# Optimization experiments

Hardware: AMD Instinct MI355X
Metric: run time of the kernel (lower is better)

Reference implementation:

```python
import jax, jax.numpy as jnp
import numpy as np


def setup_inputs() -> dict:
    key = jax.random.key(0)
    k1, k2 = jax.random.split(key)
    B, L, V, D = 8, 2048, 1024, 1024
    hidden_states = jax.random.normal(k1, (B, L, D), dtype=jnp.float32)
    visual_hidden_state = jax.random.normal(k2, (B, V, D), dtype=jnp.float32)
    return {"hidden_states": hidden_states, "visual_hidden_state": visual_hidden_state}


def reference(hidden_states, visual_hidden_state):
    # fusion_scores = H @ V^T  (no scaling, no masking)
    scores = jnp.einsum("bld,bvd->blv", hidden_states, visual_hidden_state)
    probs = jax.nn.softmax(scores, axis=-1)
    # fusion_output = probs @ V
    return jnp.einsum("blv,bvd->bld", probs, visual_hidden_state)
```

## Files before the change

### kernel.cpp

```cpp
#include <hip/hip_runtime.h>


typedef _Float16 half8_t __attribute__((ext_vector_type(8)));
typedef _Float16 half4_t __attribute__((ext_vector_type(4)));
typedef __fp16   fp16x2  __attribute__((ext_vector_type(2)));
typedef float    f32x4   __attribute__((ext_vector_type(4)));

#define B_ 8
#define L_ 2048
#define V_ 1024
#define D_ 1024

__device__ __forceinline__ half8_t cvt8(f32x4 a, f32x4 b) {
  union { half8_t h; fp16x2 p[4]; } u;
  u.p[0] = __builtin_amdgcn_cvt_pkrtz(a[0], a[1]);
  u.p[1] = __builtin_amdgcn_cvt_pkrtz(a[2], a[3]);
  u.p[2] = __builtin_amdgcn_cvt_pkrtz(b[0], b[1]);
  u.p[3] = __builtin_amdgcn_cvt_pkrtz(b[2], b[3]);
  return u.h;
}
__device__ __forceinline__ half4_t cvt4(f32x4 a) {
  union { half4_t h; fp16x2 p[2]; } u;
  u.p[0] = __builtin_amdgcn_cvt_pkrtz(a[0], a[1]);
  u.p[1] = __builtin_amdgcn_cvt_pkrtz(a[2], a[3]);
  return u.h;
}

__device__ __forceinline__ void gload_lds16(const _Float16* g, _Float16* l) {
  __builtin_amdgcn_global_load_lds(
      (const __attribute__((address_space(1))) unsigned int*)(g),
      (__attribute__((address_space(3))) unsigned int*)(l), 16, 0, 0);
}

__global__ __launch_bounds__(256) void p0_hconv(const float* __restrict__ H,
                                                _Float16* __restrict__ Hh) {
  const size_t i = ((size_t)blockIdx.x * 256 + threadIdx.x) * 8;
  f32x4 a = *(const f32x4*)(H + i);
  f32x4 b = *(const f32x4*)(H + i + 4);
  *(half8_t*)(Hh + i) = cvt8(a, b);
}

__global__ __launch_bounds__(256) void p1_vconv(const float* __restrict__ V,
                                                _Float16* __restrict__ Vh,
                                                _Float16* __restrict__ VTh) {
  const int b  = blockIdx.z;
  const int d0 = blockIdx.x * 64;
  const int v0 = blockIdx.y * 64;
  const float* Vb = V + (size_t)b * V_ * D_;
  __shared__ __align__(16) _Float16 Lt[64 * 80];
  const int t   = threadIdx.x;
  const int dc4 = (t & 15) * 4;
  #pragma unroll
  for (int it = 0; it < 4; ++it) {
    const int vr = (t >> 4) + it * 16;
    f32x4 x = *(const f32x4*)(Vb + (size_t)(v0 + vr) * D_ + d0 + dc4);
    half4_t h = cvt4(x);
    *(half4_t*)(Vh + (size_t)b * V_ * D_ + (size_t)(v0 + vr) * D_ + d0 + dc4) = h;
    #pragma unroll
    for (int j = 0; j < 4; ++j) Lt[(dc4 + j) * 80 + vr] = h[j];
  }
  __syncthreads();
  #pragma unroll
  for (int it = 0; it < 2; ++it) {
    const int dr = (t >> 3) + it * 32;
    const int vc = (t & 7) * 8;
    half8_t y = *(const half8_t*)&Lt[dr * 80 + vc];
    *(half8_t*)(VTh + (size_t)b * D_ * V_ + (size_t)(d0 + dr) * V_ + v0 + vc) = y;
  }
}

#define PH_BAR() asm volatile("s_barrier" ::: "memory")

__global__ __launch_bounds__(512, 2) void gemm256(
    const _Float16* __restrict__ A, const _Float16* __restrict__ B,
    float* __restrict__ C) {
  int lin = blockIdx.x;
  lin = (lin & 7) * 32 + (lin >> 3);
  const int bz = lin >> 5;
  const int my = (lin >> 2) & 7;
  const int nx = lin & 3;
  const int m0 = my * 256, n0 = nx * 256;

  const _Float16* Ap = A + (size_t)bz * (2048 * 1024) + (size_t)m0 * 1024;
  const _Float16* Bp = B + (size_t)bz * (1024 * 1024) + (size_t)n0 * 1024;
  float*          Cp = C + (size_t)bz * (2048 * 1024);

  __shared__ __align__(16) _Float16 As[2][16384];
  __shared__ __align__(16) _Float16 Bs[2][16384];

  const int t    = threadIdx.x;
  const int lane = t & 63;
  const int wid  = t >> 6;
  const int wm   = wid >> 2;
  const int wn   = wid & 3;
  const int fr   = lane & 15;
  const int fk   = lane >> 4;

  f32x4 acc[8][4];
  {
    f32x4 z = {0.f, 0.f, 0.f, 0.f};
    #pragma unroll
    for (int i = 0; i < 8; ++i)
      #pragma unroll
      for (int j = 0; j < 4; ++j) acc[i][j] = z;
  }

  #define STG(PTR, ARR, BUFL, H, KTT)                                          \
    {                                                                          \
      _Pragma("unroll")                                                        \
      for (int i_ = 0; i_ < 2; ++i_) {                                         \
        const int c_ = i_ * 512 + t;                                           \
        const int kg_ = c_ >> 7, r_ = c_ & 127;                                \
        gload_lds16(PTR + (size_t)((H) * 128 + r_) * 1024 + (KTT) * 64 + kg_ * 8, \
                    &ARR[BUFL][(kg_ * 256 + (H) * 128 + r_) * 8]);             \
      }                                                                        \
    }

  #define LDA(BUFL, mt_, ks_) \
    (*(const half8_t*)&As[BUFL][(((ks_) * 4 + fk) * 256 + wm * 128 + (mt_) * 16 + fr) * 8])
  #define LDB(BUFL, nt_, ks_) \
    (*(const half8_t*)&Bs[BUFL][(((ks_) * 4 + fk) * 256 + wn * 64 + (nt_) * 16 + fr) * 8])

  #define MFMA16(AF, BF, MOFF, NOFF)                                           \
    __builtin_amdgcn_s_setprio(1);                                             \
    _Pragma("unroll")                                                          \
    for (int ks = 0; ks < 2; ++ks)                                             \
      _Pragma("unroll")                                                        \
      for (int nt = 0; nt < 2; ++nt)                                           \
        _Pragma("unroll")                                                      \
        for (int mt = 0; mt < 4; ++mt)                                         \
          acc[(MOFF) + mt][(NOFF) + nt] =                                      \
              __builtin_amdgcn_mfma_f32_16x16x32_f16(                          \
                  AF[mt][ks], BF[nt][ks], acc[(MOFF) + mt][(NOFF) + nt], 0, 0, 0); \
    __builtin_amdgcn_s_setprio(0);

  #define TILE(KT, BUFL)                                                       \
    {                                                                          \
      half8_t a[4][2], b0[2][2], b1[2][2];                                     \
                         \
      _Pragma("unroll")                                                        \
      for (int ks = 0; ks < 2; ++ks) {                                         \
        _Pragma("unroll")                                                      \
        for (int mt = 0; mt < 4; ++mt) a[mt][ks] = LDA(BUFL, mt, ks);          \
        _Pragma("unroll")                                                      \
        for (int nt = 0; nt < 2; ++nt) b0[nt][ks] = LDB(BUFL, nt, ks);         \
      }                                                                        \
      PH_BAR();                                                                \
      MFMA16(a, b0, 0, 0)                                                      \
      PH_BAR();                                                                \
                   \
      _Pragma("unroll")                                                        \
      for (int ks = 0; ks < 2; ++ks)                                           \
        _Pragma("unroll")                                                      \
        for (int nt = 0; nt < 2; ++nt) b1[nt][ks] = LDB(BUFL, 2 + nt, ks);     \
      if ((KT) < 14) { STG(Bp, Bs, BUFL, 0, (KT) + 2) }                        \
      PH_BAR();                                                                \
      MFMA16(a, b1, 0, 2)                                                      \
      PH_BAR();                                                                \
                   \
      _Pragma("unroll")                                                        \
      for (int ks = 0; ks < 2; ++ks)                                           \
        _Pragma("unroll")                                                      \
        for (int mt = 0; mt < 4; ++mt) a[mt][ks] = LDA(BUFL, 4 + mt, ks);      \
      if ((KT) < 14) { STG(Bp, Bs, BUFL, 1, (KT) + 2) }                        \
      PH_BAR();                                                                \
      MFMA16(a, b1, 4, 2)                                                      \
      PH_BAR();                                                                \
                \
      if ((KT) < 14) { STG(Ap, As, BUFL, 0, (KT) + 2) STG(Ap, As, BUFL, 1, (KT) + 2) } \
      PH_BAR();                                                                \
      MFMA16(a, b0, 4, 0)                                                      \
      if ((KT) <= 13) {                                                        \
        asm volatile("s_waitcnt vmcnt(8)" ::: "memory");                       \
      } else if ((KT) == 14) {                                                 \
        asm volatile("s_waitcnt vmcnt(0)" ::: "memory");                       \
      }                                                                        \
      PH_BAR();                                                                \
    }

  STG(Bp, Bs, 0, 0, 0) STG(Ap, As, 0, 0, 0) STG(Bp, Bs, 0, 1, 0) STG(Ap, As, 0, 1, 0)
  STG(Bp, Bs, 1, 0, 1) STG(Ap, As, 1, 0, 1) STG(Bp, Bs, 1, 1, 1) STG(Ap, As, 1, 1, 1)
  asm volatile("s_waitcnt vmcnt(8)" ::: "memory");
  PH_BAR();

  #pragma unroll 1
  for (int ktp = 0; ktp < 8; ++ktp) {
    TILE(2 * ktp, 0)
    TILE(2 * ktp + 1, 1)
  }
  #undef TILE
  #undef STG
  #undef LDA
  #undef LDB
  #undef MFMA16

  const int rq = (lane >> 4) * 4;
  const int cb = n0 + wn * 64 + (lane & 15);
  const int rb = m0 + wm * 128 + rq;
  #pragma unroll
  for (int mt = 0; mt < 8; ++mt)
    #pragma unroll
    for (int nt = 0; nt < 4; ++nt) {
      #pragma unroll
      for (int r = 0; r < 4; ++r)
        Cp[(size_t)(rb + mt * 16 + r) * 1024 + cb + nt * 16] = acc[mt][nt][r];
    }
}

__global__ __launch_bounds__(256) void k2_softmax(const float* __restrict__ S,
                                                  _Float16* __restrict__ P) {
  const int t    = threadIdx.x;
  const int lane = t & 63;
  const int row  = blockIdx.x * 4 + (t >> 6);
  const float* Sr = S + (size_t)row * V_;

  f32x4 s[4];
  #pragma unroll
  for (int j = 0; j < 4; ++j) s[j] = *(const f32x4*)(Sr + (lane + 64 * j) * 4);

  float m = -1e30f;
  #pragma unroll
  for (int j = 0; j < 4; ++j)
    m = fmaxf(m, fmaxf(fmaxf(s[j][0], s[j][1]), fmaxf(s[j][2], s[j][3])));
  #pragma unroll
  for (int off = 1; off < 64; off <<= 1) m = fmaxf(m, __shfl_xor(m, off, 64));

  float sum = 0.f;
  #pragma unroll
  for (int j = 0; j < 4; ++j) {
    s[j][0] = __expf(s[j][0] - m); s[j][1] = __expf(s[j][1] - m);
    s[j][2] = __expf(s[j][2] - m); s[j][3] = __expf(s[j][3] - m);
    sum += (s[j][0] + s[j][1]) + (s[j][2] + s[j][3]);
  }
  #pragma unroll
  for (int off = 1; off < 64; off <<= 1) sum += __shfl_xor(sum, off, 64);
  const float inv = 1.0f / sum;

  _Float16* Pr = P + (size_t)row * V_;
  #pragma unroll
  for (int j = 0; j < 4; ++j) {
    f32x4 e = {s[j][0] * inv, s[j][1] * inv, s[j][2] * inv, s[j][3] * inv};
    *(half4_t*)(Pr + (lane + 64 * j) * 4) = cvt4(e);
  }
}

__global__ __launch_bounds__(256, 2) void k1_slow(
    const float* __restrict__ H, const float* __restrict__ Vv, float* __restrict__ S) {
  const int b  = blockIdx.z;
  const int m0 = blockIdx.y * 128;
  const int n0 = blockIdx.x * 128;
  const float* Hb = H  + (size_t)b * L_ * D_;
  const float* Vb = Vv + (size_t)b * V_ * D_;
  float*       Sb = S  + (size_t)b * L_ * V_;
  __shared__ __align__(16) _Float16 As[2][4096];
  __shared__ __align__(16) _Float16 Bs[2][4096];
  const int t = threadIdx.x, lane = t & 63, wm = (t >> 6) >> 1, wn = (t >> 6) & 1;
  f32x4 acc[4][4];
  { f32x4 z = {0,0,0,0};
    #pragma unroll
    for (int i = 0; i < 4; ++i)
      #pragma unroll
      for (int j = 0; j < 4; ++j) acc[i][j] = z; }
  const int skg = t & 3, sm = t >> 2;
  for (int kt = 0; kt < 32; ++kt) {
    const int kbase = kt * 32 + skg * 8, buf = kt & 1;
    #pragma unroll
    for (int h = 0; h < 2; ++h) {
      const int m = sm + h * 64;
      const float* sa = Hb + (size_t)(m0 + m) * D_ + kbase;
      const float* sb = Vb + (size_t)(n0 + m) * D_ + kbase;
      const int cell = skg * 128 + (m ^ (skg * 2));
      *(half8_t*)&As[buf][cell * 8] = cvt8(*(const f32x4*)sa, *(const f32x4*)(sa + 4));
      *(half8_t*)&Bs[buf][cell * 8] = cvt8(*(const f32x4*)sb, *(const f32x4*)(sb + 4));
    }
    __syncthreads();
    const int fkg = lane >> 4, fr = lane & 15;
    half8_t af[4];
    #pragma unroll
    for (int mt = 0; mt < 4; ++mt)
      af[mt] = *(const half8_t*)&As[buf][(fkg * 128 + ((wm * 64 + mt * 16 + fr) ^ (fkg * 2))) * 8];
    #pragma unroll
    for (int nt = 0; nt < 4; ++nt) {
      half8_t bf = *(const half8_t*)&Bs[buf][(fkg * 128 + ((wn * 64 + nt * 16 + fr) ^ (fkg * 2))) * 8];
      #pragma unroll
      for (int mt = 0; mt < 4; ++mt)
        acc[mt][nt] = __builtin_amdgcn_mfma_f32_16x16x32_f16(af[mt], bf, acc[mt][nt], 0, 0, 0);
    }
  }
  const int rq = (lane >> 4) * 4;
  #pragma unroll
  for (int mt = 0; mt < 4; ++mt)
    #pragma unroll
    for (int nt = 0; nt < 4; ++nt) {
      const int col = n0 + wn * 64 + nt * 16 + (lane & 15);
      const int rb  = m0 + wm * 64 + mt * 16 + rq;
      #pragma unroll
      for (int r = 0; r < 4; ++r) Sb[(size_t)(rb + r) * V_ + col] = acc[mt][nt][r];
    }
}

__global__ __launch_bounds__(256) void k2_slow(float* __restrict__ S) {
  const int row = blockIdx.x;
  float* Sr = S + (size_t)row * V_;
  const int t = threadIdx.x;
  f32x4 s = ((const f32x4*)Sr)[t];
  float m = fmaxf(fmaxf(s[0], s[1]), fmaxf(s[2], s[3]));
  #pragma unroll
  for (int off = 1; off < 64; off <<= 1) m = fmaxf(m, __shfl_xor(m, off, 64));
  __shared__ float redm[4];
  __shared__ float reds[4];
  const int w = t >> 6;
  if ((t & 63) == 0) redm[w] = m;
  __syncthreads();
  m = fmaxf(fmaxf(redm[0], redm[1]), fmaxf(redm[2], redm[3]));
  const float e0 = __expf(s[0] - m), e1 = __expf(s[1] - m);
  const float e2 = __expf(s[2] - m), e3 = __expf(s[3] - m);
  float sum = (e0 + e1) + (e2 + e3);
  #pragma unroll
  for (int off = 1; off < 64; off <<= 1) sum += __shfl_xor(sum, off, 64);
  if ((t & 63) == 0) reds[w] = sum;
  __syncthreads();
  const float inv = 1.0f / ((reds[0] + reds[1]) + (reds[2] + reds[3]));
  half4_t p;
  p[0] = (_Float16)(e0 * inv); p[1] = (_Float16)(e1 * inv);
  p[2] = (_Float16)(e2 * inv); p[3] = (_Float16)(e3 * inv);
  *(half4_t*)((_Float16*)Sr + 4 * t) = p;
}

__global__ __launch_bounds__(512, 2) void k3_slow(
    const float* __restrict__ Vv, float* __restrict__ O) {
  const int b = blockIdx.y, r0 = blockIdx.x * 64;
  const float* Vb = Vv + (size_t)b * V_ * D_;
  float*       Ob = O  + (size_t)b * L_ * D_;
  const _Float16* Pb = (const _Float16*)Ob;
  __shared__ __align__(16) _Float16 Bs[32768];
  const int t = threadIdx.x, lane = t & 63, w = t >> 6;
  f32x4 acc[4][8];
  { f32x4 z = {0,0,0,0};
    #pragma unroll
    for (int i = 0; i < 4; ++i)
      #pragma unroll
      for (int j = 0; j < 8; ++j) acc[i][j] = z; }
  for (int kt = 0; kt < 32; ++kt) {
    const int v0 = kt * 32;
    #pragma unroll
    for (int i = 0; i < 8; ++i) {
      const int c = t + i * 512, kg = c >> 10, d = c & 1023;
      const float* src = Vb + (size_t)(v0 + kg * 8) * D_ + d;
      f32x4 x0, x1;
      x0[0] = src[0*D_]; x0[1] = src[1*D_]; x0[2] = src[2*D_]; x0[3] = src[3*D_];
      x1[0] = src[4*D_]; x1[1] = src[5*D_]; x1[2] = src[6*D_]; x1[3] = src[7*D_];
      *(half8_t*)&Bs[(kg * 1024 + d) * 8] = cvt8(x0, x1);
    }
    __syncthreads();
    const int fkg = lane >> 4, fr = lane & 15;
    half8_t af[4];
    #pragma unroll
    for (int mt = 0; mt < 4; ++mt)
      af[mt] = *(const half8_t*)(Pb + (size_t)(r0 + mt * 16 + fr) * 2048 + v0 + fkg * 8);
    #pragma unroll
    for (int nt = 0; nt < 8; ++nt) {
      half8_t bf = *(const half8_t*)&Bs[(fkg * 1024 + w * 128 + nt * 16 + fr) * 8];
      #pragma unroll
      for (int mt = 0; mt < 4; ++mt)
        acc[mt][nt] = __builtin_amdgcn_mfma_f32_16x16x32_f16(af[mt], bf, acc[mt][nt], 0, 0, 0);
    }
    __syncthreads();
  }
  const int rq = (lane >> 4) * 4;
  #pragma unroll
  for (int mt = 0; mt < 4; ++mt)
    #pragma unroll
    for (int nt = 0; nt < 8; ++nt) {
      const int col = w * 128 + nt * 16 + (lane & 15);
      const int rb  = r0 + mt * 16 + rq;
      #pragma unroll
      for (int r = 0; r < 4; ++r) Ob[(size_t)(rb + r) * D_ + col] = acc[mt][nt][r];
    }
}

extern "C" void kernel_launch(void* const* d_in, const int* in_sizes, int n_in,
                              void* d_out, int out_size, void* d_ws, size_t ws_size,
                              hipStream_t stream) {
  (void)in_sizes; (void)n_in; (void)out_size;
  const float* H  = (const float*)d_in[0];
  const float* Vv = (const float*)d_in[1];
  float* O = (float*)d_out;

  const size_t need = (size_t)64 * 1024 * 1024;
  if (ws_size >= need && d_ws != nullptr) {
    _Float16* Hh  = (_Float16*)d_ws;
    _Float16* Vh  = Hh + (size_t)B_ * L_ * D_;
    _Float16* VTh = Vh + (size_t)B_ * V_ * D_;
    _Float16* P   = Hh;

    p0_hconv<<<dim3((B_ * L_ * D_) / (256 * 8)), 256, 0, stream>>>(H, Hh);
    p1_vconv<<<dim3(D_ / 64, V_ / 64, B_), 256, 0, stream>>>(Vv, Vh, VTh);
    gemm256<<<dim3(256), 512, 0, stream>>>(Hh, Vh, O);
    k2_softmax<<<dim3(B_ * L_ / 4), 256, 0, stream>>>(O, P);
    gemm256<<<dim3(256), 512, 0, stream>>>(P, VTh, O);
  } else {
    k1_slow<<<dim3(V_ / 128, L_ / 128, B_), 256, 0, stream>>>(H, Vv, O);
    k2_slow<<<dim3(B_ * L_), 256, 0, stream>>>(O);
    k3_slow<<<dim3(L_ / 64, B_), 512, 0, stream>>>(Vv, O);
  }
}
```

Measured before the change: 255.0 us.

## Prefetch next k-tile LDS fragments, stage GEMM epilogue via LDS, merge conversion kernels

Restructures the GEMM main loop so the A-low and B0 fragments for the next k-tile are read from the other LDS buffer during the current tile, with ping-pong register sets and sched_barriers so LDS reads overlap MFMA work. It also loosens the vmcnt wait. The epilogue now stages accumulators through LDS and writes C with coalesced 16-byte row stores instead of scattered scalar stores. The two fp32-to-fp16 conversion kernels are merged into one launch to save a kernel launch. The cost is higher register pressure from the extra fragment sets and added barriers in the epilogue.

New measurement: 284.4 us. 11.5% more time.

```diff
diff --git a/kernel.cpp b/kernel.cpp
--- a/kernel.cpp
+++ b/kernel.cpp
@@ -32,23 +32,25 @@
       (__attribute__((address_space(3))) unsigned int*)(l), 16, 0, 0);
 }
 
-__global__ __launch_bounds__(256) void p0_hconv(const float* __restrict__ H,
-                                                _Float16* __restrict__ Hh) {
-  const size_t i = ((size_t)blockIdx.x * 256 + threadIdx.x) * 8;
-  f32x4 a = *(const f32x4*)(H + i);
-  f32x4 b = *(const f32x4*)(H + i + 4);
-  *(half8_t*)(Hh + i) = cvt8(a, b);
-}
-
-__global__ __launch_bounds__(256) void p1_vconv(const float* __restrict__ V,
+__global__ __launch_bounds__(256) void p01_conv(const float* __restrict__ H,
+                                                _Float16* __restrict__ Hh,
+                                                const float* __restrict__ V,
                                                 _Float16* __restrict__ Vh,
                                                 _Float16* __restrict__ VTh) {
-  const int b  = blockIdx.z;
-  const int d0 = blockIdx.x * 64;
-  const int v0 = blockIdx.y * 64;
+  const int t = threadIdx.x;
+  if (blockIdx.x < 8192) {
+    const size_t i = ((size_t)blockIdx.x * 256 + t) * 8;
+    f32x4 a = *(const f32x4*)(H + i);
+    f32x4 b = *(const f32x4*)(H + i + 4);
+    *(half8_t*)(Hh + i) = cvt8(a, b);
+    return;
+  }
+  const int lin = blockIdx.x - 8192;
+  const int b   = lin >> 8;
+  const int d0  = (lin & 15) * 64;
+  const int v0  = ((lin >> 4) & 15) * 64;
   const float* Vb = V + (size_t)b * V_ * D_;
   __shared__ __align__(16) _Float16 Lt[64 * 80];
-  const int t   = threadIdx.x;
   const int dc4 = (t & 15) * 4;
   #pragma unroll
   for (int it = 0; it < 4; ++it) {
@@ -68,8 +70,6 @@
     *(half8_t*)(VTh + (size_t)b * D_ * V_ + (size_t)(d0 + dr) * V_ + v0 + vc) = y;
   }
 }
-
-#define PH_BAR() asm volatile("s_barrier" ::: "memory")
 
 __global__ __launch_bounds__(512, 2) void gemm256(
     const _Float16* __restrict__ A, const _Float16* __restrict__ B,
@@ -134,59 +134,70 @@
                   AF[mt][ks], BF[nt][ks], acc[(MOFF) + mt][(NOFF) + nt], 0, 0, 0); \
     __builtin_amdgcn_s_setprio(0);
 
-  #define TILE(KT, BUFL)                                                       \
+  half8_t aLo[4][2], aHi[4][2], b1[2][2], b0A[2][2], b0B[2][2];
+
+  #define TILE(KT, BUFL, OTH, B0C, B0N)                                        \
     {                                                                          \
-      half8_t a[4][2], b0[2][2], b1[2][2];                                     \
-                         \
-      _Pragma("unroll")                                                        \
-      for (int ks = 0; ks < 2; ++ks) {                                         \
-        _Pragma("unroll")                                                      \
-        for (int mt = 0; mt < 4; ++mt) a[mt][ks] = LDA(BUFL, mt, ks);          \
-        _Pragma("unroll")                                                      \
-        for (int nt = 0; nt < 2; ++nt) b0[nt][ks] = LDB(BUFL, nt, ks);         \
-      }                                                                        \
-      PH_BAR();                                                                \
-      MFMA16(a, b0, 0, 0)                                                      \
-      PH_BAR();                                                                \
-                   \
+                                 \
       _Pragma("unroll")                                                        \
       for (int ks = 0; ks < 2; ++ks)                                           \
         _Pragma("unroll")                                                      \
         for (int nt = 0; nt < 2; ++nt) b1[nt][ks] = LDB(BUFL, 2 + nt, ks);     \
-      if ((KT) < 14) { STG(Bp, Bs, BUFL, 0, (KT) + 2) }                        \
-      PH_BAR();                                                                \
-      MFMA16(a, b1, 0, 2)                                                      \
-      PH_BAR();                                                                \
-                   \
+      __builtin_amdgcn_sched_barrier(0);                                       \
+      MFMA16(aLo, B0C, 0, 0)                                                   \
+      __builtin_amdgcn_s_barrier();                                            \
+                      \
       _Pragma("unroll")                                                        \
       for (int ks = 0; ks < 2; ++ks)                                           \
         _Pragma("unroll")                                                      \
-        for (int mt = 0; mt < 4; ++mt) a[mt][ks] = LDA(BUFL, 4 + mt, ks);      \
+        for (int mt = 0; mt < 4; ++mt) aHi[mt][ks] = LDA(BUFL, 4 + mt, ks);    \
+      if ((KT) < 14) { STG(Bp, Bs, BUFL, 0, (KT) + 2) }                        \
+      __builtin_amdgcn_sched_barrier(0);                                       \
+      MFMA16(aLo, b1, 0, 2)                                                    \
+      __builtin_amdgcn_s_barrier();                                            \
+                       \
       if ((KT) < 14) { STG(Bp, Bs, BUFL, 1, (KT) + 2) }                        \
-      PH_BAR();                                                                \
-      MFMA16(a, b1, 4, 2)                                                      \
-      PH_BAR();                                                                \
-                \
+      __builtin_amdgcn_sched_barrier(0);                                       \
+      MFMA16(aHi, b1, 4, 2)                                                    \
+      if ((KT) == 14) {                                                        \
+        asm volatile("s_waitcnt vmcnt(0)" ::: "memory");                       \
+      } else if ((KT) < 14) {                                                  \
+        asm volatile("s_waitcnt vmcnt(4)" ::: "memory");                       \
+      }                                                                        \
+      __builtin_amdgcn_s_barrier();                                            \
+             \
+      if ((KT) < 15) {                                                         \
+        _Pragma("unroll")                                                      \
+        for (int ks = 0; ks < 2; ++ks) {                                       \
+          _Pragma("unroll")                                                    \
+          for (int mt = 0; mt < 4; ++mt) aLo[mt][ks] = LDA(OTH, mt, ks);       \
+          _Pragma("unroll")                                                    \
+          for (int nt = 0; nt < 2; ++nt) B0N[nt][ks] = LDB(OTH, nt, ks);       \
+        }                                                                      \
+      }                                                                        \
       if ((KT) < 14) { STG(Ap, As, BUFL, 0, (KT) + 2) STG(Ap, As, BUFL, 1, (KT) + 2) } \
-      PH_BAR();                                                                \
-      MFMA16(a, b0, 4, 0)                                                      \
-      if ((KT) <= 13) {                                                        \
-        asm volatile("s_waitcnt vmcnt(8)" ::: "memory");                       \
-      } else if ((KT) == 14) {                                                 \
-        asm volatile("s_waitcnt vmcnt(0)" ::: "memory");                       \
-      }                                                                        \
-      PH_BAR();                                                                \
+      __builtin_amdgcn_sched_barrier(0);                                       \
+      MFMA16(aHi, B0C, 4, 0)                                                   \
+      __builtin_amdgcn_s_barrier();                                            \
     }
 
   STG(Bp, Bs, 0, 0, 0) STG(Ap, As, 0, 0, 0) STG(Bp, Bs, 0, 1, 0) STG(Ap, As, 0, 1, 0)
   STG(Bp, Bs, 1, 0, 1) STG(Ap, As, 1, 0, 1) STG(Bp, Bs, 1, 1, 1) STG(Ap, As, 1, 1, 1)
   asm volatile("s_waitcnt vmcnt(8)" ::: "memory");
-  PH_BAR();
+  __builtin_amdgcn_s_barrier();
+  #pragma unroll
+  for (int ks = 0; ks < 2; ++ks) {
+    #pragma unroll
+    for (int mt = 0; mt < 4; ++mt) aLo[mt][ks] = LDA(0, mt, ks);
+    #pragma unroll
+    for (int nt = 0; nt < 2; ++nt) b0A[nt][ks] = LDB(0, nt, ks);
+  }
 
   #pragma unroll 1
-  for (int ktp = 0; ktp < 8; ++ktp) {
-    TILE(2 * ktp, 0)
-    TILE(2 * ktp + 1, 1)
+  for (int tp = 0; tp < 8; ++tp) {
+    const int kt = tp * 2;
+    TILE(kt, 0, 1, b0A, b0B)
+    TILE(kt + 1, 1, 0, b0B, b0A)
   }
   #undef TILE
   #undef STG
@@ -195,16 +206,26 @@
   #undef MFMA16
 
   const int rq = (lane >> 4) * 4;
-  const int cb = n0 + wn * 64 + (lane & 15);
-  const int rb = m0 + wm * 128 + rq;
-  #pragma unroll
-  for (int mt = 0; mt < 8; ++mt)
-    #pragma unroll
-    for (int nt = 0; nt < 4; ++nt) {
-      #pragma unroll
-      for (int r = 0; r < 4; ++r)
-        Cp[(size_t)(rb + mt * 16 + r) * 1024 + cb + nt * 16] = acc[mt][nt][r];
-    }
+  float* reg = (wid < 4) ? ((float*)As + wid * 4096)
+                         : ((float*)Bs + (wid - 4) * 4096);
+  #pragma unroll
+  for (int h = 0; h < 2; ++h) {
+    __syncthreads();
+    #pragma unroll
+    for (int mt = 0; mt < 4; ++mt)
+      #pragma unroll
+      for (int nt = 0; nt < 4; ++nt)
+        #pragma unroll
+        for (int r = 0; r < 4; ++r)
+          reg[(mt * 16 + rq + r) * 64 + nt * 16 + fr] = acc[h * 4 + mt][nt][r];
+    __syncthreads();
+    #pragma unroll
+    for (int rr = 0; rr < 16; ++rr) {
+      f32x4 v = *(const f32x4*)&reg[(rr * 4 + fk) * 64 + fr * 4];
+      const int row = m0 + wm * 128 + h * 64 + rr * 4 + fk;
+      *(f32x4*)&Cp[(size_t)row * 1024 + n0 + wn * 64 + fr * 4] = v;
+    }
+  }
 }
 
 __global__ __launch_bounds__(256) void k2_softmax(const float* __restrict__ S,
@@ -394,8 +415,7 @@
     _Float16* VTh = Vh + (size_t)B_ * V_ * D_;
     _Float16* P   = Hh;
 
-    p0_hconv<<<dim3((B_ * L_ * D_) / (256 * 8)), 256, 0, stream>>>(H, Hh);
-    p1_vconv<<<dim3(D_ / 64, V_ / 64, B_), 256, 0, stream>>>(Vv, Vh, VTh);
+    p01_conv<<<dim3(8192 + 2048), 256, 0, stream>>>(H, Hh, Vv, Vh, VTh);
     gemm256<<<dim3(256), 512, 0, stream>>>(Hh, Vh, O);
     k2_softmax<<<dim3(B_ * L_ / 4), 256, 0, stream>>>(O, P);
     gemm256<<<dim3(256), 512, 0, stream>>>(P, VTh, O);
```

## Fuse conversion, both GEMMs and softmax into one persistent kernel with grid barriers

Applied to the files above, without the earlier changes.

Replaces five separate launches (H conversion, V conversion/transpose, GEMM, softmax, GEMM) with a single persistent 256-block kernel that runs each phase in turn, separated by atomic-counter grid barriers. The aim is to remove launch gaps and per-kernel tail effects. In exchange it adds global spin barriers and a memset of the barrier counters before every launch. It also relies on all 256 blocks being co-resident, and softmax and conversion now run on only 256 blocks instead of many small ones.

Result: slower. 498.0 us (+95.3%).

```diff
diff --git a/kernel.cpp b/kernel.cpp
--- a/kernel.cpp
+++ b/kernel.cpp
@@ -10,6 +10,8 @@
 #define L_ 2048
 #define V_ 1024
 #define D_ 1024
+
+__device__ unsigned g_bar[4];
 
 __device__ __forceinline__ half8_t cvt8(f32x4 a, f32x4 b) {
   union { half8_t h; fp16x2 p[4]; } u;
@@ -32,63 +34,74 @@
       (__attribute__((address_space(3))) unsigned int*)(l), 16, 0, 0);
 }
 
-__global__ __launch_bounds__(256) void p0_hconv(const float* __restrict__ H,
-                                                _Float16* __restrict__ Hh) {
-  const size_t i = ((size_t)blockIdx.x * 256 + threadIdx.x) * 8;
-  f32x4 a = *(const f32x4*)(H + i);
-  f32x4 b = *(const f32x4*)(H + i + 4);
-  *(half8_t*)(Hh + i) = cvt8(a, b);
-}
-
-__global__ __launch_bounds__(256) void p1_vconv(const float* __restrict__ V,
-                                                _Float16* __restrict__ Vh,
-                                                _Float16* __restrict__ VTh) {
-  const int b  = blockIdx.z;
-  const int d0 = blockIdx.x * 64;
-  const int v0 = blockIdx.y * 64;
-  const float* Vb = V + (size_t)b * V_ * D_;
-  __shared__ __align__(16) _Float16 Lt[64 * 80];
+__device__ __forceinline__ void gsync(int idx) {
+  __syncthreads();
+  if (threadIdx.x == 0) {
+    __threadfence();
+    unsigned arrived = __hip_atomic_fetch_add(
+        &g_bar[idx], 1u, __ATOMIC_ACQ_REL, __HIP_MEMORY_SCOPE_AGENT) + 1u;
+    if (arrived < 256u) {
+      while (__hip_atomic_load(&g_bar[idx], __ATOMIC_ACQUIRE,
+                               __HIP_MEMORY_SCOPE_AGENT) < 256u)
+        __builtin_amdgcn_s_sleep(2);
+    }
+    __threadfence();
+  }
+  __syncthreads();
+}
+
+__global__ __launch_bounds__(512, 2) void mega(
+    const float* __restrict__ H, const float* __restrict__ Vv,
+    float* __restrict__ O, _Float16* __restrict__ Hh,
+    _Float16* __restrict__ Vh, _Float16* __restrict__ VTh) {
+  __shared__ __align__(16) _Float16 As[2][16384];
+  __shared__ __align__(16) _Float16 Bs[2][16384];
+
   const int t   = threadIdx.x;
-  const int dc4 = (t & 15) * 4;
-  #pragma unroll
-  for (int it = 0; it < 4; ++it) {
-    const int vr = (t >> 4) + it * 16;
-    f32x4 x = *(const f32x4*)(Vb + (size_t)(v0 + vr) * D_ + d0 + dc4);
-    half4_t h = cvt4(x);
-    *(half4_t*)(Vh + (size_t)b * V_ * D_ + (size_t)(v0 + vr) * D_ + d0 + dc4) = h;
-    #pragma unroll
-    for (int j = 0; j < 4; ++j) Lt[(dc4 + j) * 80 + vr] = h[j];
-  }
-  __syncthreads();
-  #pragma unroll
-  for (int it = 0; it < 2; ++it) {
-    const int dr = (t >> 3) + it * 32;
-    const int vc = (t & 7) * 8;
-    half8_t y = *(const half8_t*)&Lt[dr * 80 + vc];
-    *(half8_t*)(VTh + (size_t)b * D_ * V_ + (size_t)(d0 + dr) * V_ + v0 + vc) = y;
-  }
-}
-
-#define PH_BAR() asm volatile("s_barrier" ::: "memory")
-
-__global__ __launch_bounds__(512, 2) void gemm256(
-    const _Float16* __restrict__ A, const _Float16* __restrict__ B,
-    float* __restrict__ C) {
-  int lin = blockIdx.x;
+  const int bid = blockIdx.x;
+
+  #pragma unroll 4
+  for (int it = 0; it < 16; ++it) {
+    const size_t i = (((size_t)it * 256 + bid) * 512 + t) * 8;
+    f32x4 a = *(const f32x4*)(H + i);
+    f32x4 b = *(const f32x4*)(H + i + 4);
+    *(half8_t*)(Hh + i) = cvt8(a, b);
+  }
+  {
+    _Float16* Lt = &As[0][0];
+    const int dc4 = (t & 15) * 4;
+    for (int tt = 0; tt < 8; ++tt) {
+      const int lin = bid * 8 + tt;
+      const int b   = lin >> 8;
+      const int d0  = (lin & 15) * 64;
+      const int v0  = ((lin >> 4) & 15) * 64;
+      const float* Vb = Vv + (size_t)b * V_ * D_;
+      __syncthreads();
+      #pragma unroll
+      for (int it = 0; it < 2; ++it) {
+        const int vr = (t >> 4) + it * 32;
+        f32x4 x = *(const f32x4*)(Vb + (size_t)(v0 + vr) * D_ + d0 + dc4);
+        half4_t h = cvt4(x);
+        *(half4_t*)(Vh + (size_t)b * V_ * D_ + (size_t)(v0 + vr) * D_ + d0 + dc4) = h;
+        #pragma unroll
+        for (int j = 0; j < 4; ++j) Lt[(dc4 + j) * 80 + vr] = h[j];
+      }
+      __syncthreads();
+      const int dr = t >> 3;
+      const int vc = (t & 7) * 8;
+      half8_t y = *(const half8_t*)&Lt[dr * 80 + vc];
+      *(half8_t*)(VTh + (size_t)b * D_ * V_ + (size_t)(d0 + dr) * V_ + v0 + vc) = y;
+    }
+  }
+  gsync(0);
+
+  int lin = bid;
   lin = (lin & 7) * 32 + (lin >> 3);
   const int bz = lin >> 5;
   const int my = (lin >> 2) & 7;
   const int nx = lin & 3;
   const int m0 = my * 256, n0 = nx * 256;
 
-  const _Float16* Ap = A + (size_t)bz * (2048 * 1024) + (size_t)m0 * 1024;
-  const _Float16* Bp = B + (size_t)bz * (1024 * 1024) + (size_t)n0 * 1024;
-  float*          Cp = C + (size_t)bz * (2048 * 1024);
-
-  __shared__ __align__(16) _Float16 As[2][16384];
-  __shared__ __align__(16) _Float16 Bs[2][16384];
-
-  const int t    = threadIdx.x;
   const int lane = t & 63;
   const int wid  = t >> 6;
   const int wm   = wid >> 2;
@@ -96,31 +109,20 @@
   const int fr   = lane & 15;
   const int fk   = lane >> 4;
 
-  f32x4 acc[8][4];
-  {
-    f32x4 z = {0.f, 0.f, 0.f, 0.f};
-    #pragma unroll
-    for (int i = 0; i < 8; ++i)
-      #pragma unroll
-      for (int j = 0; j < 4; ++j) acc[i][j] = z;
-  }
-
-  #define STG(PTR, ARR, BUFL, H, KTT)                                          \
+  #define STG(PTR, ARR, BUFL, HH, KTT)                                         \
     {                                                                          \
       _Pragma("unroll")                                                        \
       for (int i_ = 0; i_ < 2; ++i_) {                                         \
         const int c_ = i_ * 512 + t;                                           \
         const int kg_ = c_ >> 7, r_ = c_ & 127;                                \
-        gload_lds16(PTR + (size_t)((H) * 128 + r_) * 1024 + (KTT) * 64 + kg_ * 8, \
-                    &ARR[BUFL][(kg_ * 256 + (H) * 128 + r_) * 8]);             \
+        gload_lds16(PTR + (size_t)((HH) * 128 + r_) * 1024 + (KTT) * 64 + kg_ * 8, \
+                    &ARR[BUFL][(kg_ * 256 + (HH) * 128 + r_) * 8]);            \
       }                                                                        \
     }
-
   #define LDA(BUFL, mt_, ks_) \
     (*(const half8_t*)&As[BUFL][(((ks_) * 4 + fk) * 256 + wm * 128 + (mt_) * 16 + fr) * 8])
   #define LDB(BUFL, nt_, ks_) \
     (*(const half8_t*)&Bs[BUFL][(((ks_) * 4 + fk) * 256 + wn * 64 + (nt_) * 16 + fr) * 8])
-
   #define MFMA16(AF, BF, MOFF, NOFF)                                           \
     __builtin_amdgcn_s_setprio(1);                                             \
     _Pragma("unroll")                                                          \
@@ -133,11 +135,9 @@
               __builtin_amdgcn_mfma_f32_16x16x32_f16(                          \
                   AF[mt][ks], BF[nt][ks], acc[(MOFF) + mt][(NOFF) + nt], 0, 0, 0); \
     __builtin_amdgcn_s_setprio(0);
-
   #define TILE(KT, BUFL)                                                       \
     {                                                                          \
       half8_t a[4][2], b0[2][2], b1[2][2];                                     \
-                         \
       _Pragma("unroll")                                                        \
       for (int ks = 0; ks < 2; ++ks) {                                         \
         _Pragma("unroll")                                                      \
@@ -145,103 +145,123 @@
         _Pragma("unroll")                                                      \
         for (int nt = 0; nt < 2; ++nt) b0[nt][ks] = LDB(BUFL, nt, ks);         \
       }                                                                        \
-      PH_BAR();                                                                \
+      __builtin_amdgcn_s_barrier();                                            \
       MFMA16(a, b0, 0, 0)                                                      \
-      PH_BAR();                                                                \
-                   \
+      __builtin_amdgcn_s_barrier();                                            \
       _Pragma("unroll")                                                        \
       for (int ks = 0; ks < 2; ++ks)                                           \
         _Pragma("unroll")                                                      \
         for (int nt = 0; nt < 2; ++nt) b1[nt][ks] = LDB(BUFL, 2 + nt, ks);     \
       if ((KT) < 14) { STG(Bp, Bs, BUFL, 0, (KT) + 2) }                        \
-      PH_BAR();                                                                \
+      __builtin_amdgcn_s_barrier();                                            \
       MFMA16(a, b1, 0, 2)                                                      \
-      PH_BAR();                                                                \
-                   \
+      __builtin_amdgcn_s_barrier();                                            \
       _Pragma("unroll")                                                        \
       for (int ks = 0; ks < 2; ++ks)                                           \
         _Pragma("unroll")                                                      \
         for (int mt = 0; mt < 4; ++mt) a[mt][ks] = LDA(BUFL, 4 + mt, ks);      \
       if ((KT) < 14) { STG(Bp, Bs, BUFL, 1, (KT) + 2) }                        \
-      PH_BAR();                                                                \
+      __builtin_amdgcn_s_barrier();                                            \
       MFMA16(a, b1, 4, 2)                                                      \
-      PH_BAR();                                                                \
-                \
+      __builtin_amdgcn_s_barrier();                                            \
       if ((KT) < 14) { STG(Ap, As, BUFL, 0, (KT) + 2) STG(Ap, As, BUFL, 1, (KT) + 2) } \
-      PH_BAR();                                                                \
+      __builtin_amdgcn_s_barrier();                                            \
       MFMA16(a, b0, 4, 0)                                                      \
       if ((KT) <= 13) {                                                        \
         asm volatile("s_waitcnt vmcnt(8)" ::: "memory");                       \
       } else if ((KT) == 14) {                                                 \
         asm volatile("s_waitcnt vmcnt(0)" ::: "memory");                       \
       }                                                                        \
-      PH_BAR();                                                                \
-    }
-
-  STG(Bp, Bs, 0, 0, 0) STG(Ap, As, 0, 0, 0) STG(Bp, Bs, 0, 1, 0) STG(Ap, As, 0, 1, 0)
-  STG(Bp, Bs, 1, 0, 1) STG(Ap, As, 1, 0, 1) STG(Bp, Bs, 1, 1, 1) STG(Ap, As, 1, 1, 1)
-  asm volatile("s_waitcnt vmcnt(8)" ::: "memory");
-  PH_BAR();
-
-  #pragma unroll 1
-  for (int ktp = 0; ktp < 8; ++ktp) {
-    TILE(2 * ktp, 0)
-    TILE(2 * ktp + 1, 1)
-  }
+      __builtin_amdgcn_s_barrier();                                            \
+    }
+
+  auto run_gemm = [&](const _Float16* __restrict__ Aall,
+                      const _Float16* __restrict__ Ball,
+                      float* __restrict__ Call) {
+    const _Float16* Ap = Aall + (size_t)bz * (2048 * 1024) + (size_t)m0 * 1024;
+    const _Float16* Bp = Ball + (size_t)bz * (1024 * 1024) + (size_t)n0 * 1024;
+    float*          Cp = Call + (size_t)bz * (2048 * 1024);
+
+    f32x4 acc[8][4];
+    {
+      f32x4 z = {0.f, 0.f, 0.f, 0.f};
+      #pragma unroll
+      for (int i = 0; i < 8; ++i)
+        #pragma unroll
+        for (int j = 0; j < 4; ++j) acc[i][j] = z;
+    }
+
+    STG(Bp, Bs, 0, 0, 0) STG(Ap, As, 0, 0, 0) STG(Bp, Bs, 0, 1, 0) STG(Ap, As, 0, 1, 0)
+    STG(Bp, Bs, 1, 0, 1) STG(Ap, As, 1, 0, 1) STG(Bp, Bs, 1, 1, 1) STG(Ap, As, 1, 1, 1)
+    asm volatile("s_waitcnt vmcnt(8)" ::: "memory");
+    __builtin_amdgcn_s_barrier();
+
+    #pragma unroll 1
+    for (int ktp = 0; ktp < 8; ++ktp) {
+      TILE(2 * ktp, 0)
+      TILE(2 * ktp + 1, 1)
+    }
+
+    const int rq = (lane >> 4) * 4;
+    #pragma unroll
+    for (int mt = 0; mt < 8; ++mt)
+      #pragma unroll
+      for (int nt = 0; nt < 4; ++nt) {
+        const int col   = n0 + wn * 64 + nt * 16 + (lane & 15);
+        const int rbase = m0 + wm * 128 + mt * 16 + rq;
+        #pragma unroll
+        for (int r = 0; r < 4; ++r)
+          Cp[(size_t)(rbase + r) * 1024 + col] = acc[mt][nt][r];
+      }
+  };
+
+  run_gemm(Hh, Vh, O);
+  gsync(1);
+
+  {
+    const int xb = bid & 7;
+    const int jb = bid >> 3;
+    _Float16* P = Hh;
+    #pragma unroll 1
+    for (int it = 0; it < 8; ++it) {
+      const int row = xb * 2048 + jb * 64 + (t >> 6) * 8 + it;
+      const float* Sr = O + (size_t)row * V_;
+      f32x4 s[4];
+      #pragma unroll
+      for (int j = 0; j < 4; ++j) s[j] = *(const f32x4*)(Sr + (lane + 64 * j) * 4);
+      float m = -1e30f;
+      #pragma unroll
+      for (int j = 0; j < 4; ++j)
+        m = fmaxf(m, fmaxf(fmaxf(s[j][0], s[j][1]), fmaxf(s[j][2], s[j][3])));
+      #pragma unroll
+      for (int off = 1; off < 64; off <<= 1) m = fmaxf(m, __shfl_xor(m, off, 64));
+      float sum = 0.f;
+      #pragma unroll
+      for (int j = 0; j < 4; ++j) {
+        s[j][0] = __expf(s[j][0] - m); s[j][1] = __expf(s[j][1] - m);
+        s[j][2] = __expf(s[j][2] - m); s[j][3] = __expf(s[j][3] - m);
+        sum += (s[j][0] + s[j][1]) + (s[j][2] + s[j][3]);
+      }
+      #pragma unroll
+      for (int off = 1; off < 64; off <<= 1) sum += __shfl_xor(sum, off, 64);
+      const float inv = 1.0f / sum;
+      _Float16* Pr = P + (size_t)row * V_;
+      #pragma unroll
+      for (int j = 0; j < 4; ++j) {
+        f32x4 e = {s[j][0] * inv, s[j][1] * inv, s[j][2] * inv, s[j][3] * inv};
+        *(half4_t*)(Pr + (lane + 64 * j) * 4) = cvt4(e);
+      }
+    }
+  }
+  gsync(2);
+
+  run_gemm(Hh , VTh, O);
+
   #undef TILE
   #undef STG
   #undef LDA
   #undef LDB
   #undef MFMA16
-
-  const int rq = (lane >> 4) * 4;
-  const int cb = n0 + wn * 64 + (lane & 15);
-  const int rb = m0 + wm * 128 + rq;
-  #pragma unroll
-  for (int mt = 0; mt < 8; ++mt)
-    #pragma unroll
-    for (int nt = 0; nt < 4; ++nt) {
-      #pragma unroll
-      for (int r = 0; r < 4; ++r)
-        Cp[(size_t)(rb + mt * 16 + r) * 1024 + cb + nt * 16] = acc[mt][nt][r];
-    }
-}
-
-__global__ __launch_bounds__(256) void k2_softmax(const float* __restrict__ S,
-                                                  _Float16* __restrict__ P) {
-  const int t    = threadIdx.x;
-  const int lane = t & 63;
-  const int row  = blockIdx.x * 4 + (t >> 6);
-  const float* Sr = S + (size_t)row * V_;
-
-  f32x4 s[4];
-  #pragma unroll
-  for (int j = 0; j < 4; ++j) s[j] = *(const f32x4*)(Sr + (lane + 64 * j) * 4);
-
-  float m = -1e30f;
-  #pragma unroll
-  for (int j = 0; j < 4; ++j)
-    m = fmaxf(m, fmaxf(fmaxf(s[j][0], s[j][1]), fmaxf(s[j][2], s[j][3])));
-  #pragma unroll
-  for (int off = 1; off < 64; off <<= 1) m = fmaxf(m, __shfl_xor(m, off, 64));
-
-  float sum = 0.f;
-  #pragma unroll
-  for (int j = 0; j < 4; ++j) {
-    s[j][0] = __expf(s[j][0] - m); s[j][1] = __expf(s[j][1] - m);
-    s[j][2] = __expf(s[j][2] - m); s[j][3] = __expf(s[j][3] - m);
-    sum += (s[j][0] + s[j][1]) + (s[j][2] + s[j][3]);
-  }
-  #pragma unroll
-  for (int off = 1; off < 64; off <<= 1) sum += __shfl_xor(sum, off, 64);
-  const float inv = 1.0f / sum;
-
-  _Float16* Pr = P + (size_t)row * V_;
-  #pragma unroll
-  for (int j = 0; j < 4; ++j) {
-    f32x4 e = {s[j][0] * inv, s[j][1] * inv, s[j][2] * inv, s[j][3] * inv};
-    *(half4_t*)(Pr + (lane + 64 * j) * 4) = cvt4(e);
-  }
 }
 
 __global__ __launch_bounds__(256, 2) void k1_slow(
@@ -392,13 +412,13 @@
     _Float16* Hh  = (_Float16*)d_ws;
     _Float16* Vh  = Hh + (size_t)B_ * L_ * D_;
     _Float16* VTh = Vh + (size_t)B_ * V_ * D_;
-    _Float16* P   = Hh;
-
-    p0_hconv<<<dim3((B_ * L_ * D_) / (256 * 8)), 256, 0, stream>>>(H, Hh);
-    p1_vconv<<<dim3(D_ / 64, V_ / 64, B_), 256, 0, stream>>>(Vv, Vh, VTh);
-    gemm256<<<dim3(256), 512, 0, stream>>>(Hh, Vh, O);
-    k2_softmax<<<dim3(B_ * L_ / 4), 256, 0, stream>>>(O, P);
-    gemm256<<<dim3(256), 512, 0, stream>>>(P, VTh, O);
+
+    static void* bar_ptr = nullptr;
+    if (bar_ptr == nullptr) {
+      (void)hipGetSymbolAddress(&bar_ptr, HIP_SYMBOL(g_bar));
+    }
+    hipMemsetAsync(bar_ptr, 0, sizeof(unsigned) * 4, stream);
+    mega<<<dim3(256), 512, 0, stream>>>(H, Vv, O, Hh, Vh, VTh);
   } else {
     k1_slow<<<dim3(V_ / 128, L_ / 128, B_), 256, 0, stream>>>(H, Vv, O);
     k2_slow<<<dim3(B_ * L_), 256, 0, stream>>>(O);
```
